# Kernel tuning notes

Hardware: AMD Instinct MI355X
Metric: run time of the kernel (lower is better)

## Reference

```python
import jax, jax.numpy as jnp
import numpy as np

# Module constants (from init_kwargs)
SEED_H = 32
SEED_W = 32
SEED_LEVEL = 4
EPS = 1e-8
OFFSETS = [(-1, -1), (-1, 0), (-1, 1), (0, -1), (0, 0), (0, 1), (1, -1), (1, 0), (1, 1)]


def setup_inputs() -> dict:
    key = jax.random.key(0)
    x = jax.random.normal(key, (8, 20, 512, 512), dtype=jnp.float32)
    return {"input": x}


def _seg_sum(vals, idx, num_segments):
    # vals: [B, HW] or [B, HW, C]; idx: [HW]
    return jax.vmap(lambda v: jax.ops.segment_sum(v, idx, num_segments=num_segments))(vals)


def _lattice_superpixel(x):
    B, C, H, W = x.shape
    ch, cw = H // SEED_H, W // SEED_W          # seed cell size
    S = SEED_H * SEED_W                        # number of seeds
    HW = H * W

    # initial seeds: mean of each lattice cell -> [B, C, SEED_H, SEED_W]
    seeds = x.reshape(B, C, SEED_H, ch, SEED_W, cw).mean(axis=(3, 5))

    # pixel -> candidate seed flat indices for the 3x3 seed neighborhood
    ph = jnp.arange(H) // ch                   # [H] seed row of each pixel
    pw = jnp.arange(W) // cw                   # [W] seed col of each pixel
    idxs = []
    for dy, dx in OFFSETS:
        iy = jnp.clip(ph + dy, 0, SEED_H - 1)
        ix = jnp.clip(pw + dx, 0, SEED_W - 1)
        idxs.append((iy[:, None] * SEED_W + ix[None, :]).reshape(-1))  # [HW]
    idxs = jnp.stack(idxs)                     # [9, HW]

    xp = x.transpose(0, 2, 3, 1).reshape(B, HW, C)  # pixel features [B, HW, C]

    Q = None
    for _ in range(SEED_LEVEL):
        # pixel-to-seed squared distances over the 9 candidate seeds
        sflat = seeds.reshape(B, C, S).transpose(0, 2, 1)  # [B, S, C]
        dists = []
        for o in range(9):
            s_o = sflat[:, idxs[o], :]                      # [B, HW, C]
            dists.append(jnp.sum((xp - s_o) ** 2, axis=-1))  # [B, HW]
        dist = jnp.stack(dists, axis=1)                     # [B, 9, HW]
        Q = jax.nn.softmax(-dist, axis=1)                   # soft associations

        # seed update: weighted mean of associated pixel features
        numer = jnp.zeros((B, S, C), x.dtype)
        denom = jnp.zeros((B, S), x.dtype)
        for o in range(9):
            w = Q[:, o, :]                                  # [B, HW]
            numer = numer + _seg_sum(w[..., None] * xp, idxs[o], S)
            denom = denom + _seg_sum(w, idxs[o], S)
        seeds = (numer / (denom[..., None] + EPS)).transpose(0, 2, 1).reshape(B, C, SEED_H, SEED_W)

    return Q.reshape(B, 9, H, W)


def reference(input) -> jnp.ndarray:
    return _lattice_superpixel(input)
```

## Files before the change

kernel.cpp:

```cpp
#include <hip/hip_runtime.h>

#define NB 8
#define NC 20
#define NH 512
#define NW 512
#define NS 1024
#define HW (NH * NW)
#define SEEDS_ELEMS (NB * NS * NC)
#define SNORM_ELEMS (NB * NS)
#define PART_STRIDE 189
#define EPSF 1e-8f

static constexpr int DYO[9] = {-1, -1, -1, 0, 0, 0, 1, 1, 1};
static constexpr int DXO[9] = {-1, 0, 1, -1, 0, 1, -1, 0, 1};

__device__ __forceinline__ int clampi(int v, int lo, int hi) {
    return v < lo ? lo : (v > hi ? hi : v);
}

__device__ __forceinline__ int xcd_cell(int bx) {
    return ((bx & 7) << 7) + (bx >> 3);
}

__global__ __launch_bounds__(160) void k_seed_init(const float* __restrict__ x,
                                                   float* __restrict__ seeds,
                                                   float* __restrict__ snorm) {
    __shared__ float sm[NC];
    const int tt = threadIdx.x;
    const int cell = blockIdx.x;
    const int b = blockIdx.y;
    const int cy = cell >> 5, cx = cell & 31;
    const int c = tt >> 3, s = tt & 7;

    const float* xb = x + (size_t)b * (NC * HW) + (size_t)c * HW
                        + (size_t)(cy << 4) * NW + (cx << 4);
    float acc = 0.f;
#pragma unroll
    for (int k = 0; k < 8; ++k) {
        const int row = (k << 1) + (s >> 2);
        const int col = (s & 3) << 2;
        const float4 v = *reinterpret_cast<const float4*>(xb + row * NW + col);
        acc += v.x + v.y + v.z + v.w;
    }
    acc += __shfl_xor(acc, 1, 64);
    acc += __shfl_xor(acc, 2, 64);
    acc += __shfl_xor(acc, 4, 64);
    if (s == 0) {
        const float mv = acc * (1.0f / 256.0f);
        seeds[((size_t)(b << 10) + cell) * NC + c] = mv;
        sm[c] = mv;
    }
    __syncthreads();
    if (tt == 0) {
        float n = 0.f;
#pragma unroll
        for (int cc = 0; cc < NC; ++cc) n += sm[cc] * sm[cc];
        snorm[(b << 10) + cell] = n;
    }
}

__global__ __launch_bounds__(256, 4) void k_iter(const float* __restrict__ x,
                                                 const float* __restrict__ seeds,
                                                 const float* __restrict__ snorm,
                                                 float* __restrict__ part) {
    __shared__ __align__(16) float qs[9 * 256];
    __shared__ float pbuf[4 * 9 * 24];

    const int t = threadIdx.x;
    const int cell = xcd_cell(blockIdx.x);
    const int b = blockIdx.y;
    const int cy = cell >> 5, cx = cell & 31;

    const float* xb = x + (size_t)b * (NC * HW) + (size_t)(cy << 4) * NW + (cx << 4);

    const float* xp = xb + (t >> 4) * NW + (t & 15);
    float xv[NC];
#pragma unroll
    for (int c = 0; c < NC; ++c) xv[c] = xp[(size_t)c * HW];

    float d[9];
#pragma unroll
    for (int o = 0; o < 9; ++o) {
        const int ny = clampi(cy + DYO[o], 0, 31);
        const int nx = clampi(cx + DXO[o], 0, 31);
        const int si = __builtin_amdgcn_readfirstlane((b << 10) + (ny << 5) + nx);
        const float* sp = seeds + (size_t)si * NC;
        float ip = 0.f;
#pragma unroll
        for (int c = 0; c < NC; ++c) ip += xv[c] * sp[c];
        d[o] = snorm[si] - 2.0f * ip;
    }
    float m = d[0];
#pragma unroll
    for (int o = 1; o < 9; ++o) m = fminf(m, d[o]);
    float w[9];
    float wsum = 0.f;
#pragma unroll
    for (int o = 0; o < 9; ++o) {
        w[o] = __expf(m - d[o]);
        wsum += w[o];
    }
    const float inv = 1.0f / wsum;
#pragma unroll
    for (int o = 0; o < 9; ++o) qs[(o << 8) + t] = w[o] * inv;
    __syncthreads();

    const int wid = t >> 6, tl = t & 63;
    if (tl < 56) {
        const int cg = tl >> 3, s = tl & 7;
        const int r0 = cg * 3;
        float acc[3][9];
#pragma unroll
        for (int j = 0; j < 3; ++j)
#pragma unroll
            for (int o = 0; o < 9; ++o) acc[j][o] = 0.f;

#pragma unroll
        for (int kk = 0; kk < 2; ++kk) {
            const int q = (((wid << 1) + kk) << 3) + s;
            const float* xr = xb + (q >> 2) * NW + ((q & 3) << 2);
            const float4 x0 = *reinterpret_cast<const float4*>(xr + (size_t)(r0 + 0) * HW);
            const float4 x1 = *reinterpret_cast<const float4*>(xr + (size_t)(r0 + 1) * HW);
            float4 x2 = make_float4(1.f, 1.f, 1.f, 1.f);
            if (cg < 6)
                x2 = *reinterpret_cast<const float4*>(xr + (size_t)(r0 + 2) * HW);
#pragma unroll
            for (int o = 0; o < 9; ++o) {
                const float4 q4 = *reinterpret_cast<const float4*>(&qs[(o << 8) + (q << 2)]);
                acc[0][o] += q4.x * x0.x + q4.y * x0.y + q4.z * x0.z + q4.w * x0.w;
                acc[1][o] += q4.x * x1.x + q4.y * x1.y + q4.z * x1.z + q4.w * x1.w;
                acc[2][o] += q4.x * x2.x + q4.y * x2.y + q4.z * x2.z + q4.w * x2.w;
            }
        }
#pragma unroll
        for (int j = 0; j < 3; ++j)
#pragma unroll
            for (int o = 0; o < 9; ++o) {
                acc[j][o] += __shfl_xor(acc[j][o], 1, 64);
                acc[j][o] += __shfl_xor(acc[j][o], 2, 64);
                acc[j][o] += __shfl_xor(acc[j][o], 4, 64);
            }
        if (s == 0) {
#pragma unroll
            for (int o = 0; o < 9; ++o)
#pragma unroll
                for (int j = 0; j < 3; ++j)
                    pbuf[wid * 216 + o * 24 + r0 + j] = acc[j][o];
        }
    }
    __syncthreads();

    if (t < PART_STRIDE) {
        const int o = t / 21, c = t - o * 21;
        const float v = pbuf[o * 24 + c] + pbuf[216 + o * 24 + c]
                      + pbuf[432 + o * 24 + c] + pbuf[648 + o * 24 + c];
        part[(size_t)((b << 10) + cell) * PART_STRIDE + t] = v;
    }
}

__global__ __launch_bounds__(192) void k_divz(const float* __restrict__ part,
                                              float* __restrict__ seeds,
                                              float* __restrict__ snorm) {
    __shared__ float den[8];
    __shared__ float sq[8][20];
    const int t = threadIdx.x;
    const int sl = t / 21, c = t - sl * 21;
    const int sid = blockIdx.x * 8 + sl;

    float tot = 0.f;
    if (t < 168) {
        const int b = sid >> 10;
        const int s1 = sid & 1023;
        const int sy = s1 >> 5, sx = s1 & 31;

        int cys[3], dys[3], cxs[3], dxs[3];
        cys[0] = sy > 0 ? sy - 1 : 0;   dys[0] = (sy == 0) ? -1 : 1;
        cys[1] = sy;                    dys[1] = 0;
        cys[2] = sy < 31 ? sy + 1 : 31; dys[2] = (sy == 31) ? 1 : -1;
        cxs[0] = sx > 0 ? sx - 1 : 0;   dxs[0] = (sx == 0) ? -1 : 1;
        cxs[1] = sx;                    dxs[1] = 0;
        cxs[2] = sx < 31 ? sx + 1 : 31; dxs[2] = (sx == 31) ? 1 : -1;

#pragma unroll
        for (int jy = 0; jy < 3; ++jy)
#pragma unroll
            for (int jx = 0; jx < 3; ++jx) {
                const int cell = (b << 10) + (cys[jy] << 5) + cxs[jx];
                const int o = (dys[jy] + 1) * 3 + (dxs[jx] + 1);
                tot += part[(size_t)cell * PART_STRIDE + o * 21 + c];
            }
        if (c == 20) den[sl] = tot;
    }
    __syncthreads();
    if (t < 168 && c < 20) {
        const float v = tot / (den[sl] + EPSF);
        seeds[(size_t)sid * NC + c] = v;
        sq[sl][c] = v * v;
    }
    __syncthreads();
    if (t < 8) {
        float n = 0.f;
#pragma unroll
        for (int cc = 0; cc < NC; ++cc) n += sq[t][cc];
        snorm[blockIdx.x * 8 + t] = n;
    }
}

__global__ __launch_bounds__(256, 4) void k_final4(const float* __restrict__ x,
                                                   const float* __restrict__ seeds,
                                                   const float* __restrict__ snorm,
                                                   float* __restrict__ out) {
    __shared__ __align__(16) float s_all[3][6][20];
    __shared__ float s_n[3][6];

    const int t = threadIdx.x;
    const int grp = ((blockIdx.x & 7) << 5) + (blockIdx.x >> 3);
    const int b = blockIdx.y;
    const int cy = grp >> 3, cxg = grp & 7;

    if (t < 180) {
#pragma unroll
        for (int ee = 0; ee < 2; ++ee) {
            const int e = t + ee * 180;
            const int srow = e / 120;
            const int rem = e - srow * 120;
            const int scol = rem / 20;
            const int c = rem - scol * 20;
            const int sy = clampi(cy + srow - 1, 0, 31);
            const int sx = clampi((cxg << 2) + scol - 1, 0, 31);
            s_all[srow][scol][c] =
                seeds[((size_t)((b << 10) + (sy << 5) + sx)) * NC + c];
        }
    }
    if (t < 18) {
        const int srow = t / 6, scol = t - srow * 6;
        const int sy = clampi(cy + srow - 1, 0, 31);
        const int sx = clampi((cxg << 2) + scol - 1, 0, 31);
        s_n[srow][scol] = snorm[(b << 10) + (sy << 5) + sx];
    }
    __syncthreads();

    const int r = t >> 4, g = t & 15;
    const int q = g >> 2;
    const int py = (cy << 4) + r;
    const int px = (cxg << 6) + (g << 2);
    const float* xp = x + (size_t)b * (NC * HW) + (size_t)py * NW + px;

    float4 ip[9];
#pragma unroll
    for (int o = 0; o < 9; ++o) ip[o] = make_float4(0.f, 0.f, 0.f, 0.f);

#pragma unroll
    for (int j = 0; j < 5; ++j) {
        float4 xc[4];
#pragma unroll
        for (int cc = 0; cc < 4; ++cc)
            xc[cc] = *reinterpret_cast<const float4*>(xp + (size_t)((j << 2) + cc) * HW);
#pragma unroll
        for (int o = 0; o < 9; ++o) {
            const float4 s4 = *reinterpret_cast<const float4*>(
                &s_all[DYO[o] + 1][q + DXO[o] + 1][j << 2]);
            ip[o].x += xc[0].x * s4.x + xc[1].x * s4.y + xc[2].x * s4.z + xc[3].x * s4.w;
            ip[o].y += xc[0].y * s4.x + xc[1].y * s4.y + xc[2].y * s4.z + xc[3].y * s4.w;
            ip[o].z += xc[0].z * s4.x + xc[1].z * s4.y + xc[2].z * s4.z + xc[3].z * s4.w;
            ip[o].w += xc[0].w * s4.x + xc[1].w * s4.y + xc[2].w * s4.z + xc[3].w * s4.w;
        }
    }

#pragma unroll
    for (int o = 0; o < 9; ++o) {
        const float sn = s_n[DYO[o] + 1][q + DXO[o] + 1];
        ip[o].x = sn - 2.0f * ip[o].x;
        ip[o].y = sn - 2.0f * ip[o].y;
        ip[o].z = sn - 2.0f * ip[o].z;
        ip[o].w = sn - 2.0f * ip[o].w;
    }
    float4 m = ip[0];
#pragma unroll
    for (int o = 1; o < 9; ++o) {
        m.x = fminf(m.x, ip[o].x);
        m.y = fminf(m.y, ip[o].y);
        m.z = fminf(m.z, ip[o].z);
        m.w = fminf(m.w, ip[o].w);
    }
    float4 ws = make_float4(0.f, 0.f, 0.f, 0.f);
#pragma unroll
    for (int o = 0; o < 9; ++o) {
        ip[o].x = __expf(m.x - ip[o].x);
        ip[o].y = __expf(m.y - ip[o].y);
        ip[o].z = __expf(m.z - ip[o].z);
        ip[o].w = __expf(m.w - ip[o].w);
        ws.x += ip[o].x; ws.y += ip[o].y; ws.z += ip[o].z; ws.w += ip[o].w;
    }
    const float4 inv = make_float4(1.0f / ws.x, 1.0f / ws.y, 1.0f / ws.z, 1.0f / ws.w);
#pragma unroll
    for (int o = 0; o < 9; ++o) {
        const float4 v = make_float4(ip[o].x * inv.x, ip[o].y * inv.y,
                                     ip[o].z * inv.z, ip[o].w * inv.w);
        *reinterpret_cast<float4*>(
            &out[(((size_t)b * 9 + o) * NH + py) * NW + px]) = v;
    }
}

extern "C" void kernel_launch(void* const* d_in, const int* in_sizes, int n_in,
                              void* d_out, int out_size, void* d_ws, size_t ws_size,
                              hipStream_t stream) {
    const float* x = (const float*)d_in[0];
    float* out = (float*)d_out;

    float* seeds = (float*)d_ws;
    float* snorm = seeds + SEEDS_ELEMS;
    float* part  = snorm + SNORM_ELEMS;

    const dim3 grid(NS, NB);
    k_seed_init<<<grid, 160, 0, stream>>>(x, seeds, snorm);

    for (int it = 0; it < 3; ++it) {
        k_iter<<<grid, 256, 0, stream>>>(x, seeds, snorm, part);
        k_divz<<<NB * NS / 8, 192, 0, stream>>>(part, seeds, snorm);
    }
    k_final4<<<dim3(256, NB), 256, 0, stream>>>(x, seeds, snorm, out);
}
```

Before: 441.0 us.

## Process two seed cells per block with shared-memory seed staging in iteration kernel

Result: slower. 607.3 us (+37.7%).

```diff
diff --git a/kernel.cpp b/kernel.cpp
--- a/kernel.cpp
+++ b/kernel.cpp
@@ -18,10 +18,6 @@
     return v < lo ? lo : (v > hi ? hi : v);
 }
 
-__device__ __forceinline__ int xcd_cell(int bx) {
-    return ((bx & 7) << 7) + (bx >> 3);
-}
-
 __global__ __launch_bounds__(160) void k_seed_init(const float* __restrict__ x,
                                                    float* __restrict__ seeds,
                                                    float* __restrict__ snorm) {
@@ -59,53 +55,98 @@
     }
 }
 
-__global__ __launch_bounds__(256, 4) void k_iter(const float* __restrict__ x,
-                                                 const float* __restrict__ seeds,
-                                                 const float* __restrict__ snorm,
-                                                 float* __restrict__ part) {
-    __shared__ __align__(16) float qs[9 * 256];
-    __shared__ float pbuf[4 * 9 * 24];
+__global__ __launch_bounds__(256, 4) void k_iter2(const float* __restrict__ x,
+                                                  const float* __restrict__ seeds,
+                                                  const float* __restrict__ snorm,
+                                                  float* __restrict__ part) {
+    __shared__ __align__(16) float qs[9][512];
+    __shared__ __align__(16) float s_all[3][4][20];
+    __shared__ float s_n[3][4];
+    __shared__ float pbuf[2][2][192];
 
     const int t = threadIdx.x;
-    const int cell = xcd_cell(blockIdx.x);
+    const int grp = ((blockIdx.x & 7) << 6) + (blockIdx.x >> 3);
     const int b = blockIdx.y;
-    const int cy = cell >> 5, cx = cell & 31;
-
-    const float* xb = x + (size_t)b * (NC * HW) + (size_t)(cy << 4) * NW + (cx << 4);
-
-    const float* xp = xb + (t >> 4) * NW + (t & 15);
-    float xv[NC];
-#pragma unroll
-    for (int c = 0; c < NC; ++c) xv[c] = xp[(size_t)c * HW];
-
-    float d[9];
-#pragma unroll
-    for (int o = 0; o < 9; ++o) {
-        const int ny = clampi(cy + DYO[o], 0, 31);
-        const int nx = clampi(cx + DXO[o], 0, 31);
-        const int si = __builtin_amdgcn_readfirstlane((b << 10) + (ny << 5) + nx);
-        const float* sp = seeds + (size_t)si * NC;
-        float ip = 0.f;
-#pragma unroll
-        for (int c = 0; c < NC; ++c) ip += xv[c] * sp[c];
-        d[o] = snorm[si] - 2.0f * ip;
-    }
-    float m = d[0];
-#pragma unroll
-    for (int o = 1; o < 9; ++o) m = fminf(m, d[o]);
-    float w[9];
-    float wsum = 0.f;
-#pragma unroll
-    for (int o = 0; o < 9; ++o) {
-        w[o] = __expf(m - d[o]);
-        wsum += w[o];
-    }
-    const float inv = 1.0f / wsum;
-#pragma unroll
-    for (int o = 0; o < 9; ++o) qs[(o << 8) + t] = w[o] * inv;
-    __syncthreads();
-
-    const int wid = t >> 6, tl = t & 63;
+    const int cy = grp >> 4, cxg = grp & 15;
+    const int cell0 = (cy << 5) + (cxg << 1);
+
+    const float* xb = x + (size_t)b * (NC * HW) + (size_t)(cy << 4) * NW + (cxg << 5);
+
+    const int r = t >> 4, g = t & 15;
+    const int q = g >> 3;
+    const float* xp = xb + r * NW + (g << 1);
+    float2 xv[NC];
+#pragma unroll
+    for (int c = 0; c < NC; ++c)
+        xv[c] = *reinterpret_cast<const float2*>(xp + (size_t)c * HW);
+
+    if (t < 120) {
+#pragma unroll
+        for (int ee = 0; ee < 2; ++ee) {
+            const int e = t + ee * 120;
+            const int srow = e / 80;
+            const int rem = e - srow * 80;
+            const int scol = rem / 20;
+            const int c = rem - scol * 20;
+            const int sy = clampi(cy + srow - 1, 0, 31);
+            const int sx = clampi((cxg << 1) + scol - 1, 0, 31);
+            s_all[srow][scol][c] =
+                seeds[((size_t)((b << 10) + (sy << 5) + sx)) * NC + c];
+        }
+    }
+    if (t < 12) {
+        const int srow = t >> 2, scol = t & 3;
+        const int sy = clampi(cy + srow - 1, 0, 31);
+        const int sx = clampi((cxg << 1) + scol - 1, 0, 31);
+        s_n[srow][scol] = snorm[(b << 10) + (sy << 5) + sx];
+    }
+    __syncthreads();
+
+    float2 ip[9];
+#pragma unroll
+    for (int o = 0; o < 9; ++o) ip[o] = make_float2(0.f, 0.f);
+#pragma unroll
+    for (int j = 0; j < 5; ++j) {
+#pragma unroll
+        for (int o = 0; o < 9; ++o) {
+            const float4 s4 = *reinterpret_cast<const float4*>(
+                &s_all[DYO[o] + 1][q + DXO[o] + 1][j << 2]);
+            const float2 x0 = xv[(j << 2) + 0], x1 = xv[(j << 2) + 1];
+            const float2 x2 = xv[(j << 2) + 2], x3 = xv[(j << 2) + 3];
+            ip[o].x += x0.x * s4.x + x1.x * s4.y + x2.x * s4.z + x3.x * s4.w;
+            ip[o].y += x0.y * s4.x + x1.y * s4.y + x2.y * s4.z + x3.y * s4.w;
+        }
+    }
+#pragma unroll
+    for (int o = 0; o < 9; ++o) {
+        const float sn = s_n[DYO[o] + 1][q + DXO[o] + 1];
+        ip[o].x = sn - 2.0f * ip[o].x;
+        ip[o].y = sn - 2.0f * ip[o].y;
+    }
+    float2 m = ip[0];
+#pragma unroll
+    for (int o = 1; o < 9; ++o) {
+        m.x = fminf(m.x, ip[o].x);
+        m.y = fminf(m.y, ip[o].y);
+    }
+    float2 ws = make_float2(0.f, 0.f);
+#pragma unroll
+    for (int o = 0; o < 9; ++o) {
+        ip[o].x = __expf(m.x - ip[o].x);
+        ip[o].y = __expf(m.y - ip[o].y);
+        ws.x += ip[o].x;
+        ws.y += ip[o].y;
+    }
+    const float2 inv = make_float2(1.0f / ws.x, 1.0f / ws.y);
+#pragma unroll
+    for (int o = 0; o < 9; ++o) {
+        *reinterpret_cast<float2*>(&qs[o][(r << 5) + (g << 1)]) =
+            make_float2(ip[o].x * inv.x, ip[o].y * inv.y);
+    }
+    __syncthreads();
+
+    const int w = t >> 6, tl = t & 63;
+    const int cellL = w >> 1, half = w & 1;
     if (tl < 56) {
         const int cg = tl >> 3, s = tl & 7;
         const int r0 = cg * 3;
@@ -116,9 +157,10 @@
             for (int o = 0; o < 9; ++o) acc[j][o] = 0.f;
 
 #pragma unroll
-        for (int kk = 0; kk < 2; ++kk) {
-            const int q = (((wid << 1) + kk) << 3) + s;
-            const float* xr = xb + (q >> 2) * NW + ((q & 3) << 2);
+        for (int kk = 0; kk < 4; ++kk) {
+            const int qd = (((half << 2) + kk) << 3) + s;
+            const int row = qd >> 2, qc = qd & 3;
+            const float* xr = xb + row * NW + (cellL << 4) + (qc << 2);
             const float4 x0 = *reinterpret_cast<const float4*>(xr + (size_t)(r0 + 0) * HW);
             const float4 x1 = *reinterpret_cast<const float4*>(xr + (size_t)(r0 + 1) * HW);
             float4 x2 = make_float4(1.f, 1.f, 1.f, 1.f);
@@ -126,7 +168,8 @@
                 x2 = *reinterpret_cast<const float4*>(xr + (size_t)(r0 + 2) * HW);
 #pragma unroll
             for (int o = 0; o < 9; ++o) {
-                const float4 q4 = *reinterpret_cast<const float4*>(&qs[(o << 8) + (q << 2)]);
+                const float4 q4 = *reinterpret_cast<const float4*>(
+                    &qs[o][(row << 5) + (cellL << 4) + (qc << 2)]);
                 acc[0][o] += q4.x * x0.x + q4.y * x0.y + q4.z * x0.z + q4.w * x0.w;
                 acc[1][o] += q4.x * x1.x + q4.y * x1.y + q4.z * x1.z + q4.w * x1.w;
                 acc[2][o] += q4.x * x2.x + q4.y * x2.y + q4.z * x2.z + q4.w * x2.w;
@@ -145,16 +188,15 @@
             for (int o = 0; o < 9; ++o)
 #pragma unroll
                 for (int j = 0; j < 3; ++j)
-                    pbuf[wid * 216 + o * 24 + r0 + j] = acc[j][o];
-        }
-    }
-    __syncthreads();
-
-    if (t < PART_STRIDE) {
-        const int o = t / 21, c = t - o * 21;
-        const float v = pbuf[o * 24 + c] + pbuf[216 + o * 24 + c]
-                      + pbuf[432 + o * 24 + c] + pbuf[648 + o * 24 + c];
-        part[(size_t)((b << 10) + cell) * PART_STRIDE + t] = v;
+                    pbuf[cellL][half][o * 21 + r0 + j] = acc[j][o];
+        }
+    }
+    __syncthreads();
+
+    const size_t pbase = (size_t)((b << 10) + cell0) * PART_STRIDE;
+    for (int i = t; i < 2 * PART_STRIDE; i += 256) {
+        const int cl = i / PART_STRIDE, idx = i - cl * PART_STRIDE;
+        part[pbase + i] = pbuf[cl][0][idx] + pbuf[cl][1][idx];
     }
 }
 
@@ -312,11 +354,11 @@
     float* snorm = seeds + SEEDS_ELEMS;
     float* part  = snorm + SNORM_ELEMS;
 
-    const dim3 grid(NS, NB);
-    k_seed_init<<<grid, 160, 0, stream>>>(x, seeds, snorm);
+    const dim3 gseed(NS, NB);
+    k_seed_init<<<gseed, 160, 0, stream>>>(x, seeds, snorm);
 
     for (int it = 0; it < 3; ++it) {
-        k_iter<<<grid, 256, 0, stream>>>(x, seeds, snorm, part);
+        k_iter2<<<dim3(512, NB), 256, 0, stream>>>(x, seeds, snorm, part);
         k_divz<<<NB * NS / 8, 192, 0, stream>>>(part, seeds, snorm);
     }
     k_final4<<<dim3(256, NB), 256, 0, stream>>>(x, seeds, snorm, out);
```
